# Kernel tuning notes

Measured on AMD Instinct MI355X. Metric: run time of the kernel, lower is better.

The kernel has to match this reference:

```python
import jax, jax.numpy as jnp
import numpy as np

EPS = 1e-5

def _bn_train(h, gamma, beta):
    # BatchNorm1d in training mode: batch mean and biased variance over batch dim
    mu = jnp.mean(h, axis=0)
    var = jnp.mean((h - mu) ** 2, axis=0)
    return (h - mu) * jax.lax.rsqrt(var + EPS) * gamma + beta

def setup_inputs() -> dict:
    key = jax.random.key(0)
    ks = jax.random.split(key, 12)
    B, IN, H1, H2, NC = 16384, 4096, 256, 128, 12
    x = jax.random.normal(ks[0], (B, 1, 64, 64), dtype=jnp.float32)
    y = jax.random.randint(ks[1], (B,), 0, NC, dtype=jnp.int32)
    s1 = 1.0 / np.sqrt(IN)
    W1 = jax.random.uniform(ks[2], (H1, IN), jnp.float32, -s1, s1)
    b1 = jax.random.uniform(ks[3], (H1,), jnp.float32, -s1, s1)
    g1 = jax.random.normal(ks[4], (H1,), jnp.float32) * 0.1 + 1.0
    be1 = jax.random.normal(ks[5], (H1,), jnp.float32) * 0.1
    s2 = 1.0 / np.sqrt(H1)
    W2 = jax.random.uniform(ks[6], (H2, H1), jnp.float32, -s2, s2)
    b2 = jax.random.uniform(ks[7], (H2,), jnp.float32, -s2, s2)
    g2 = jax.random.normal(ks[8], (H2,), jnp.float32) * 0.1 + 1.0
    be2 = jax.random.normal(ks[9], (H2,), jnp.float32) * 0.1
    s4 = 1.0 / np.sqrt(H2)
    W4 = jax.random.uniform(ks[10], (NC, H2), jnp.float32, -s4, s4)
    b4 = jax.random.uniform(ks[11], (NC,), jnp.float32, -s4, s4)
    return {"x": x, "W1": W1, "b1": b1, "g1": g1, "be1": be1,
            "W2": W2, "b2": b2, "g2": g2, "be2": be2,
            "W4": W4, "b4": b4, "y": y}

def reference(x, W1, b1, g1, be1, W2, b2, g2, be2, W4, b4, y):
    B = x.shape[0]
    h = x.reshape(B, -1)  # [B, 4096]
    # layer 1: binarized linear + BN(train) + hardtanh (dropout p=0 is identity)
    h = h @ jnp.sign(W1).T + jnp.sign(b1)
    h = jnp.clip(_bn_train(h, g1, be1), -1.0, 1.0)
    # layer 2
    h = h @ jnp.sign(W2).T + jnp.sign(b2)
    h = jnp.clip(_bn_train(h, g2, be2), -1.0, 1.0)
    # final float linear
    return h @ W4.T + b4  # [B, 12]
```

## Files before the change

### kernel.cpp

```cpp
#include <hip/hip_runtime.h>
#include <cstddef>

typedef __attribute__((ext_vector_type(8))) short short8;
typedef __attribute__((ext_vector_type(4))) float f4;
typedef __attribute__((ext_vector_type(4))) unsigned int u4;
typedef __attribute__((ext_vector_type(2))) unsigned int u2;

__device__ __forceinline__ unsigned int f2bf(float f){
  unsigned int u = __float_as_uint(f);
  u += 0x7fffu + ((u >> 16) & 1u);
  return u >> 16;
}
__device__ __forceinline__ float bflo(unsigned int w){ return __uint_as_float((w & 0xFFFFu) << 16); }
__device__ __forceinline__ float bfhi(unsigned int w){ return __uint_as_float(w & 0xFFFF0000u); }
__device__ __forceinline__ float fsign(float x){ return (x > 0.f) ? 1.f : ((x < 0.f) ? -1.f : 0.f); }
__device__ __forceinline__ float hclip(float x){ return fminf(1.f, fmaxf(-1.f, x)); }

#define SB0 __builtin_amdgcn_sched_barrier(0)

#define BARRIER() do { \
    SB0; \
    asm volatile("s_waitcnt lgkmcnt(0)" ::: "memory"); \
    __builtin_amdgcn_s_barrier(); \
    asm volatile("" ::: "memory"); \
    SB0; \
  } while(0)

#define VBAR(N) do { \
    SB0; \
    asm volatile("s_waitcnt vmcnt(" #N ") lgkmcnt(0)" ::: "memory"); \
    __builtin_amdgcn_s_barrier(); \
    asm volatile("" ::: "memory"); \
    SB0; \
  } while(0)

#define GL16(gp, lp) __builtin_amdgcn_global_load_lds( \
    (const __attribute__((address_space(1))) void*)(gp), \
    (__attribute__((address_space(3))) void*)(lp), 16, 0, 0)

__global__ void prep_sign_k(const float* __restrict__ W1, unsigned short* __restrict__ w1s,
                            const float* __restrict__ W2, unsigned short* __restrict__ w2s){
  int i = (blockIdx.x * blockDim.x + threadIdx.x) * 8;
  const float* w; unsigned short* o; int off;
  if (i < 1048576){ w = W1; o = w1s; off = i; }
  else            { w = W2; o = w2s; off = i - 1048576; if (off >= 32768) return; }
  f4 a = *(const f4*)(w + off);
  f4 b = *(const f4*)(w + off + 4);
  unsigned short s[8];
  #pragma unroll
  for (int j = 0; j < 4; j++) s[j]   = (a[j] > 0.f) ? 0x3F80u : ((a[j] < 0.f) ? 0xBF80u : 0u);
  #pragma unroll
  for (int j = 0; j < 4; j++) s[4+j] = (b[j] > 0.f) ? 0x3F80u : ((b[j] < 0.f) ? 0xBF80u : 0u);
  u4 v;
  v.x = (unsigned)s[0] | ((unsigned)s[1] << 16);
  v.y = (unsigned)s[2] | ((unsigned)s[3] << 16);
  v.z = (unsigned)s[4] | ((unsigned)s[5] << 16);
  v.w = (unsigned)s[6] | ((unsigned)s[7] << 16);
  *(u4*)(o + off) = v;
}

__global__ __launch_bounds__(512, 4) void gemm1_k(
    const float* __restrict__ x, const unsigned short* __restrict__ w1s,
    const float* __restrict__ b1, unsigned short* __restrict__ h1,
    float* __restrict__ part1s, float* __restrict__ part1q)
{
  __shared__ __align__(16) char lds[73728];
  const int tid  = threadIdx.x;
  const int lane = tid & 63;
  const int wid  = tid >> 6;
  const int cl   = lane & 15;
  const int g    = lane >> 4;
  const int row0 = blockIdx.x * 32;

  const int am = tid >> 4;
  const int kf = (tid & 15) * 4;
  const float* xA = x + (size_t)(row0 + am) * 4096 + kf;
  const int aw = (am * 128 + kf * 2) ^ ((am & 7) << 4);

  f4 acc[2][2];
  const f4 z = {0.f, 0.f, 0.f, 0.f};
  #pragma unroll
  for (int i = 0; i < 2; i++){ acc[i][0] = z; acc[i][1] = z; }

  f4 rA0, rA1;

#define ISSUEA(S, KB) do { rA##S = *(const f4*)(xA + (KB)*64); } while(0)

#define ISSUEB(BUF, KB) do { \
    char* _dst = lds + 8192 + (BUF)*32768; \
    _Pragma("unroll") \
    for (int _c = 0; _c < 4; _c++){ \
      int _o  = _c*8192 + tid*16; \
      int _n  = _o >> 7; \
      int _kb = (_o & 127) ^ ((_n & 7) << 4); \
      GL16((const char*)w1s + (size_t)_n*8192 + (size_t)(KB)*128 + _kb, _dst + _o); \
    } } while(0)

#define PACKA(S, ABUF) do { \
    u2 _v; \
    _v.x = f2bf(rA##S[0]) | (f2bf(rA##S[1]) << 16); \
    _v.y = f2bf(rA##S[2]) | (f2bf(rA##S[3]) << 16); \
    *(u2*)(lds + (ABUF)*4096 + aw) = _v; \
  } while(0)

#define COMPUTE(BUF) do { \
    const char* _ab = lds + (BUF)*4096; \
    const char* _bb = lds + 8192 + (BUF)*32768; \
    short8 _af[2][2]; short8 _bf[2][2]; \
    _Pragma("unroll") \
    for (int fm = 0; fm < 2; fm++){ \
      int _m = fm*16 + cl; \
      _Pragma("unroll") \
      for (int ks = 0; ks < 2; ks++) \
        _af[fm][ks] = *(const short8*)(_ab + ((_m*128 + ks*64 + g*16) ^ ((_m & 7) << 4))); \
    } \
    _Pragma("unroll") \
    for (int fn = 0; fn < 2; fn++){ \
      int _n = wid*32 + fn*16 + cl; \
      _Pragma("unroll") \
      for (int ks = 0; ks < 2; ks++) \
        _bf[fn][ks] = *(const short8*)(_bb + ((_n*128 + ks*64 + g*16) ^ ((_n & 7) << 4))); \
    } \
    _Pragma("unroll") \
    for (int ks = 0; ks < 2; ks++) \
      _Pragma("unroll") \
      for (int fm = 0; fm < 2; fm++) \
        _Pragma("unroll") \
        for (int fn = 0; fn < 2; fn++) \
          acc[fm][fn] = __builtin_amdgcn_mfma_f32_16x16x32_bf16(_af[fm][ks], _bf[fn][ks], acc[fm][fn], 0, 0, 0); \
  } while(0)

  ISSUEB(0, 0);
  ISSUEA(0, 0);
  ISSUEA(1, 1);
  SB0;
  PACKA(0, 0);
  VBAR(1);

  for (int k = 0; k < 64; k += 2){
    if (k < 63) ISSUEB(1, k + 1);
    if (k < 62) ISSUEA(0, k + 2);
    SB0;
    COMPUTE(0);
    SB0;
    if (k < 63) PACKA(1, 1);
    if (k < 62)      VBAR(1);
    else if (k < 63) VBAR(0);
    if (k + 1 < 63) ISSUEB(0, k + 2);
    if (k + 1 < 62) ISSUEA(1, k + 3);
    SB0;
    COMPUTE(1);
    SB0;
    if (k + 1 < 63){ PACKA(0, 0); VBAR(1); }
  }
#undef COMPUTE
#undef PACKA
#undef ISSUEB
#undef ISSUEA

  #pragma unroll
  for (int fn = 0; fn < 2; fn++){
    int c = wid * 32 + fn * 16 + cl;
    float sb = fsign(b1[c]);
    float s = 0.f, q = 0.f;
    #pragma unroll
    for (int fm = 0; fm < 2; fm++){
      int rbase = row0 + fm * 16 + g * 4;
      #pragma unroll
      for (int i = 0; i < 4; i++){
        float v = acc[fm][fn][i] + sb;
        h1[(size_t)(rbase + i) * 256 + c] = (unsigned short)f2bf(v);
        s += v; q += v * v;
      }
    }
    s += __shfl_xor(s, 16, 64); s += __shfl_xor(s, 32, 64);
    q += __shfl_xor(q, 16, 64); q += __shfl_xor(q, 32, 64);
    if (g == 0){
      part1s[(size_t)c * 512 + blockIdx.x] = s;
      part1q[(size_t)c * 512 + blockIdx.x] = q;
    }
  }
}

template<int COLS, int NBLK>
__global__ __launch_bounds__(64) void params_k(
    const float* __restrict__ ps, const float* __restrict__ pq,
    const float* __restrict__ g, const float* __restrict__ be,
    float* __restrict__ ab){
  int j = blockIdx.x * 64 + threadIdx.x;
  const f4* vs = (const f4*)(ps + (size_t)j * NBLK);
  const f4* vq = (const f4*)(pq + (size_t)j * NBLK);
  f4 s4 = {0,0,0,0}, q4 = {0,0,0,0};
  #pragma unroll 8
  for (int b = 0; b < NBLK/4; b++){ s4 += vs[b]; q4 += vq[b]; }
  float s = s4[0]+s4[1]+s4[2]+s4[3];
  float q = q4[0]+q4[1]+q4[2]+q4[3];
  float mu  = s * (1.f/16384.f);
  float var = q * (1.f/16384.f) - mu*mu;
  float a   = g[j] * rsqrtf(var + 1e-5f);
  ab[j] = a;
  ab[COLS + j] = be[j] - mu*a;
}

__global__ __launch_bounds__(512) void gemm2_k(
    const unsigned short* __restrict__ h1, const unsigned short* __restrict__ w2s,
    const float* __restrict__ b2, const float* __restrict__ ab1,
    unsigned short* __restrict__ h2, float* __restrict__ part2s, float* __restrict__ part2q)
{
  __shared__ __align__(16) char lds[32768];
  __shared__ __align__(16) float a1l[256];
  __shared__ __align__(16) float c1l[256];
  const int tid  = threadIdx.x;
  const int lane = tid & 63;
  const int wid  = tid >> 6;
  const int cl   = lane & 15;
  const int g    = lane >> 4;
  const int klo  = g * 8;
  const int row0 = blockIdx.x * 64;

  if (tid < 256) a1l[tid] = ab1[tid];
  else           c1l[tid - 256] = ab1[tid];

  const int am  = tid >> 3;
  const int ak0 = (tid & 7) * 8;
  const unsigned short* hA = h1 + (size_t)(row0 + am) * 256 + ak0;
  const int aw = ((am * 128) + (ak0 * 2)) ^ ((am & 7) << 4);
  const unsigned short* wbase = w2s + (size_t)(wid * 16 + cl) * 256 + klo;

  u4 q0 = *(const u4*)(hA);
  u4 q1 = *(const u4*)(hA + 64);
  u4 q2 = *(const u4*)(hA + 128);
  u4 q3 = *(const u4*)(hA + 192);
  short8 Bq0, Bq1, Br0, Br1;
  Bq0 = *(const short8*)(wbase);
  Bq1 = *(const short8*)(wbase + 32);

  BARRIER();

#define TRW(KB, RAW) do { \
    f4 _a0 = *(const f4*)(&a1l[(KB)*64 + ak0]); \
    f4 _a1 = *(const f4*)(&a1l[(KB)*64 + ak0 + 4]); \
    f4 _c0 = *(const f4*)(&c1l[(KB)*64 + ak0]); \
    f4 _c1 = *(const f4*)(&c1l[(KB)*64 + ak0 + 4]); \
    float _t0 = hclip(_a0[0]*bflo(RAW.x) + _c0[0]); \
    float _t1 = hclip(_a0[1]*bfhi(RAW.x) + _c0[1]); \
    float _t2 = hclip(_a0[2]*bflo(RAW.y) + _c0[2]); \
    float _t3 = hclip(_a0[3]*bfhi(RAW.y) + _c0[3]); \
    float _t4 = hclip(_a1[0]*bflo(RAW.z) + _c1[0]); \
    float _t5 = hclip(_a1[1]*bfhi(RAW.z) + _c1[1]); \
    float _t6 = hclip(_a1[2]*bflo(RAW.w) + _c1[2]); \
    float _t7 = hclip(_a1[3]*bfhi(RAW.w) + _c1[3]); \
    u4 _v; \
    _v.x = f2bf(_t0) | (f2bf(_t1) << 16); \
    _v.y = f2bf(_t2) | (f2bf(_t3) << 16); \
    _v.z = f2bf(_t4) | (f2bf(_t5) << 16); \
    _v.w = f2bf(_t6) | (f2bf(_t7) << 16); \
    *(u4*)(lds + (KB)*8192 + aw) = _v; \
  } while(0)

  TRW(0, q0); TRW(1, q1); TRW(2, q2); TRW(3, q3);
#undef TRW
  BARRIER();

  f4 acc[4];
  const f4 z = {0.f, 0.f, 0.f, 0.f};
  #pragma unroll
  for (int i = 0; i < 4; i++) acc[i] = z;

#define LOADB2(P, KB) do { \
    B##P##0 = *(const short8*)(wbase + (KB)*64); \
    B##P##1 = *(const short8*)(wbase + (KB)*64 + 32); \
  } while(0)

#define COMP2(BASE, P) do { \
    const char* _ab = (const char*)(BASE); \
    short8 _af[4][2]; \
    _Pragma("unroll") \
    for (int fm = 0; fm < 4; fm++){ \
      int _m = fm*16 + cl; \
      _af[fm][0] = *(const short8*)(_ab + ((_m*128 + klo*2) ^ ((_m & 7) << 4))); \
      _af[fm][1] = *(const short8*)(_ab + ((_m*128 + (32 + klo)*2) ^ ((_m & 7) << 4))); \
    } \
    _Pragma("unroll") \
    for (int fm = 0; fm < 4; fm++){ \
      acc[fm] = __builtin_amdgcn_mfma_f32_16x16x32_bf16(_af[fm][0], B##P##0, acc[fm], 0, 0, 0); \
      acc[fm] = __builtin_amdgcn_mfma_f32_16x16x32_bf16(_af[fm][1], B##P##1, acc[fm], 0, 0, 0); \
    } \
  } while(0)

  LOADB2(r, 1);
  COMP2(lds,         q);
  LOADB2(q, 2);
  COMP2(lds +  8192, r);
  LOADB2(r, 3);
  COMP2(lds + 16384, q);
  COMP2(lds + 24576, r);
#undef COMP2
#undef LOADB2

  {
    int c = wid*16 + cl;
    float sb = fsign(b2[c]);
    float s = 0.f, q = 0.f;
    #pragma unroll
    for (int fm = 0; fm < 4; fm++){
      int rbase = row0 + fm*16 + g*4;
      #pragma unroll
      for (int i = 0; i < 4; i++){
        float v = acc[fm][i] + sb;
        h2[(size_t)(rbase + i)*128 + c] = (unsigned short)f2bf(v);
        s += v; q += v*v;
      }
    }
    s += __shfl_xor(s, 16, 64); s += __shfl_xor(s, 32, 64);
    q += __shfl_xor(q, 16, 64); q += __shfl_xor(q, 32, 64);
    if (g == 0){
      part2s[c*256 + blockIdx.x] = s;
      part2q[c*256 + blockIdx.x] = q;
    }
  }
}

__global__ __launch_bounds__(128) void final_k(
    const unsigned short* __restrict__ h2,
    const float* __restrict__ part2s, const float* __restrict__ part2q,
    const float* __restrict__ g2, const float* __restrict__ be2,
    const float* __restrict__ W4, const float* __restrict__ b4,
    float* __restrict__ out)
{
  __shared__ __align__(16) float W4l[12*128];
  __shared__ __align__(16) float a2l[128];
  __shared__ __align__(16) float c2l[128];
  const int t = threadIdx.x;
  #pragma unroll
  for (int i = 0; i < 3; i++)
    *(f4*)&W4l[(i*128 + t)*4] = *(const f4*)(W4 + (i*128 + t)*4);
  {
    const f4* vs = (const f4*)(part2s + t*256);
    const f4* vq = (const f4*)(part2q + t*256);
    f4 s4 = {0,0,0,0}, q4 = {0,0,0,0};
    #pragma unroll 8
    for (int b = 0; b < 64; b++){ s4 += vs[b]; q4 += vq[b]; }
    float s = s4[0]+s4[1]+s4[2]+s4[3];
    float q = q4[0]+q4[1]+q4[2]+q4[3];
    float mu  = s * (1.f/16384.f);
    float var = q * (1.f/16384.f) - mu*mu;
    float a   = g2[t] * rsqrtf(var + 1e-5f);
    a2l[t] = a;
    c2l[t] = be2[t] - mu*a;
  }
  __syncthreads();

  const int r = blockIdx.x * 128 + t;
  const u4* hp = (const u4*)(h2 + (size_t)r * 128);
  u4 hv0 = hp[0], hv1 = hp[1], hv2 = hp[2],  hv3 = hp[3];
  u4 hv4 = hp[4], hv5 = hp[5], hv6 = hp[6],  hv7 = hp[7];
  u4 hv8 = hp[8], hv9 = hp[9], hv10 = hp[10], hv11 = hp[11];
  u4 hv12 = hp[12], hv13 = hp[13], hv14 = hp[14], hv15 = hp[15];

  float acc[12];
  #pragma unroll
  for (int o = 0; o < 12; o++) acc[o] = b4[o];

#define FPROC(HV, J) do { \
    f4 a0 = *(const f4*)&a2l[(J)*8];     f4 a1 = *(const f4*)&a2l[(J)*8 + 4]; \
    f4 c0 = *(const f4*)&c2l[(J)*8];     f4 c1 = *(const f4*)&c2l[(J)*8 + 4]; \
    float tt0 = hclip(a0[0]*bflo(HV.x) + c0[0]); \
    float tt1 = hclip(a0[1]*bfhi(HV.x) + c0[1]); \
    float tt2 = hclip(a0[2]*bflo(HV.y) + c0[2]); \
    float tt3 = hclip(a0[3]*bfhi(HV.y) + c0[3]); \
    float tt4 = hclip(a1[0]*bflo(HV.z) + c1[0]); \
    float tt5 = hclip(a1[1]*bfhi(HV.z) + c1[1]); \
    float tt6 = hclip(a1[2]*bflo(HV.w) + c1[2]); \
    float tt7 = hclip(a1[3]*bfhi(HV.w) + c1[3]); \
    _Pragma("unroll") \
    for (int o = 0; o < 12; o++){ \
      f4 w0 = *(const f4*)&W4l[o*128 + (J)*8]; \
      f4 w1 = *(const f4*)&W4l[o*128 + (J)*8 + 4]; \
      acc[o] += tt0*w0[0] + tt1*w0[1] + tt2*w0[2] + tt3*w0[3] \
              + tt4*w1[0] + tt5*w1[1] + tt6*w1[2] + tt7*w1[3]; \
    } \
  } while(0)

  FPROC(hv0, 0);  FPROC(hv1, 1);  FPROC(hv2, 2);   FPROC(hv3, 3);
  FPROC(hv4, 4);  FPROC(hv5, 5);  FPROC(hv6, 6);   FPROC(hv7, 7);
  FPROC(hv8, 8);  FPROC(hv9, 9);  FPROC(hv10, 10); FPROC(hv11, 11);
  FPROC(hv12, 12); FPROC(hv13, 13); FPROC(hv14, 14); FPROC(hv15, 15);
#undef FPROC

  #pragma unroll
  for (int o = 0; o < 12; o++) out[(size_t)r*12 + o] = acc[o];
}

extern "C" void kernel_launch(void* const* d_in, const int* in_sizes, int n_in,
                              void* d_out, int out_size, void* d_ws, size_t ws_size,
                              hipStream_t stream)
{
  const float* x   = (const float*)d_in[0];
  const float* W1  = (const float*)d_in[1];
  const float* b1  = (const float*)d_in[2];
  const float* g1  = (const float*)d_in[3];
  const float* be1 = (const float*)d_in[4];
  const float* W2  = (const float*)d_in[5];
  const float* b2  = (const float*)d_in[6];
  const float* g2  = (const float*)d_in[7];
  const float* be2 = (const float*)d_in[8];
  const float* W4  = (const float*)d_in[9];
  const float* b4  = (const float*)d_in[10];
  float* out = (float*)d_out;

  char* ws = (char*)d_ws;
  unsigned short* h1     = (unsigned short*)(ws);
  unsigned short* h2     = (unsigned short*)(ws + 8388608);
  unsigned short* w1s    = (unsigned short*)(ws + 12582912);
  unsigned short* w2s    = (unsigned short*)(ws + 14680064);
  float*          part1s = (float*)(ws + 14745600);
  float*          part1q = (float*)(ws + 15269888);
  float*          part2s = (float*)(ws + 15794176);
  float*          part2q = (float*)(ws + 15925248);
  float*          ab1    = (float*)(ws + 16056320);

  prep_sign_k<<<528, 256, 0, stream>>>(W1, w1s, W2, w2s);
  gemm1_k<<<512, 512, 0, stream>>>(x, w1s, b1, h1, part1s, part1q);
  params_k<256, 512><<<4, 64, 0, stream>>>(part1s, part1q, g1, be1, ab1);
  gemm2_k<<<256, 512, 0, stream>>>(h1, w2s, b2, ab1, h2, part2s, part2q);
  final_k<<<128, 128, 0, stream>>>(h2, part2s, part2q, g2, be2, W4, b4, out);
}
```

Measured before the change: 132.8 us.

## Restructure gemm1: fp32 A via direct LDS loads, B fragments held in registers

Doubles the rows per block to 64 and splits the 8 waves into a 2x4 grid. The fp32 activations are now streamed straight into a 4-deep swizzled LDS ring and converted to bf16 at fragment-read time. Sign weights are loaded straight from global into double-buffered registers instead of going through LDS, and each stage now covers 128 of K instead of 64. The aim is to remove the per-thread register staging and pack step for A and the LDS traffic for B. The cost is heavier register pressure, lower occupancy (launch bounds drop from 4 to 2), repeated B loads across blocks, and the BN partial sums are now written per half-block.

```diff
diff --git a/kernel.cpp b/kernel.cpp
--- a/kernel.cpp
+++ b/kernel.cpp
@@ -59,113 +59,139 @@
   *(u4*)(o + off) = v;
 }
 
-__global__ __launch_bounds__(512, 4) void gemm1_k(
+__global__ __launch_bounds__(512, 2) void gemm1_k(
     const float* __restrict__ x, const unsigned short* __restrict__ w1s,
     const float* __restrict__ b1, unsigned short* __restrict__ h1,
     float* __restrict__ part1s, float* __restrict__ part1q)
 {
-  __shared__ __align__(16) char lds[73728];
+  __shared__ __align__(16) char lds[131072];
   const int tid  = threadIdx.x;
   const int lane = tid & 63;
   const int wid  = tid >> 6;
+  const int wm   = wid >> 2;
+  const int wn   = wid & 3;
   const int cl   = lane & 15;
   const int g    = lane >> 4;
-  const int row0 = blockIdx.x * 32;
-
-  const int am = tid >> 4;
-  const int kf = (tid & 15) * 4;
-  const float* xA = x + (size_t)(row0 + am) * 4096 + kf;
-  const int aw = (am * 128 + kf * 2) ^ ((am & 7) << 4);
-
-  f4 acc[2][2];
+  const int row0 = blockIdx.x * 64;
+
+  const char* bb0 = (const char*)w1s + (size_t)(wn*64 +  0 + cl) * 8192 + g * 16;
+  const char* bb1 = (const char*)w1s + (size_t)(wn*64 + 16 + cl) * 8192 + g * 16;
+  const char* bb2 = (const char*)w1s + (size_t)(wn*64 + 32 + cl) * 8192 + g * 16;
+  const char* bb3 = (const char*)w1s + (size_t)(wn*64 + 48 + cl) * 8192 + g * 16;
+
+  f4 acc[2][4];
   const f4 z = {0.f, 0.f, 0.f, 0.f};
   #pragma unroll
-  for (int i = 0; i < 2; i++){ acc[i][0] = z; acc[i][1] = z; }
-
-  f4 rA0, rA1;
-
-#define ISSUEA(S, KB) do { rA##S = *(const f4*)(xA + (KB)*64); } while(0)
-
-#define ISSUEB(BUF, KB) do { \
-    char* _dst = lds + 8192 + (BUF)*32768; \
+  for (int i = 0; i < 2; i++)
+    #pragma unroll
+    for (int j = 0; j < 4; j++) acc[i][j] = z;
+
+  short8 B0_00, B0_01, B0_02, B0_03, B0_10, B0_11, B0_12, B0_13;
+  short8 B0_20, B0_21, B0_22, B0_23, B0_30, B0_31, B0_32, B0_33;
+  short8 B1_00, B1_01, B1_02, B1_03, B1_10, B1_11, B1_12, B1_13;
+  short8 B1_20, B1_21, B1_22, B1_23, B1_30, B1_31, B1_32, B1_33;
+
+#define ISSUEB(S, K) do { \
+    const size_t _ko = (size_t)(K) * 256; \
+    B##S##_00 = *(const short8*)(bb0 + _ko +   0); \
+    B##S##_01 = *(const short8*)(bb0 + _ko +  64); \
+    B##S##_02 = *(const short8*)(bb0 + _ko + 128); \
+    B##S##_03 = *(const short8*)(bb0 + _ko + 192); \
+    B##S##_10 = *(const short8*)(bb1 + _ko +   0); \
+    B##S##_11 = *(const short8*)(bb1 + _ko +  64); \
+    B##S##_12 = *(const short8*)(bb1 + _ko + 128); \
+    B##S##_13 = *(const short8*)(bb1 + _ko + 192); \
+    B##S##_20 = *(const short8*)(bb2 + _ko +   0); \
+    B##S##_21 = *(const short8*)(bb2 + _ko +  64); \
+    B##S##_22 = *(const short8*)(bb2 + _ko + 128); \
+    B##S##_23 = *(const short8*)(bb2 + _ko + 192); \
+    B##S##_30 = *(const short8*)(bb3 + _ko +   0); \
+    B##S##_31 = *(const short8*)(bb3 + _ko +  64); \
+    B##S##_32 = *(const short8*)(bb3 + _ko + 128); \
+    B##S##_33 = *(const short8*)(bb3 + _ko + 192); \
+  } while(0)
+
+#define ISSUEA(K) do { \
+    const int _kc = (K); \
+    char* _dst = lds + (size_t)(_kc & 3) * 32768; \
     _Pragma("unroll") \
     for (int _c = 0; _c < 4; _c++){ \
-      int _o  = _c*8192 + tid*16; \
-      int _n  = _o >> 7; \
-      int _kb = (_o & 127) ^ ((_n & 7) << 4); \
-      GL16((const char*)w1s + (size_t)_n*8192 + (size_t)(KB)*128 + _kb, _dst + _o); \
+      int _o = _c * 8192 + tid * 16; \
+      int _m = _o >> 9; \
+      int _swb = (_o & 511) ^ ((_m & 7) << 4); \
+      GL16((const char*)x + (size_t)(row0 + _m) * 16384 + (size_t)_kc * 512 + _swb, _dst + _o); \
     } } while(0)
 
-#define PACKA(S, ABUF) do { \
-    u2 _v; \
-    _v.x = f2bf(rA##S[0]) | (f2bf(rA##S[1]) << 16); \
-    _v.y = f2bf(rA##S[2]) | (f2bf(rA##S[3]) << 16); \
-    *(u2*)(lds + (ABUF)*4096 + aw) = _v; \
-  } while(0)
-
-#define COMPUTE(BUF) do { \
-    const char* _ab = lds + (BUF)*4096; \
-    const char* _bb = lds + 8192 + (BUF)*32768; \
-    short8 _af[2][2]; short8 _bf[2][2]; \
+#define MF1(S, KS) \
+    acc[0][0] = __builtin_amdgcn_mfma_f32_16x16x32_bf16(af[0][KS], B##S##_0##KS, acc[0][0], 0, 0, 0); \
+    acc[0][1] = __builtin_amdgcn_mfma_f32_16x16x32_bf16(af[0][KS], B##S##_1##KS, acc[0][1], 0, 0, 0); \
+    acc[0][2] = __builtin_amdgcn_mfma_f32_16x16x32_bf16(af[0][KS], B##S##_2##KS, acc[0][2], 0, 0, 0); \
+    acc[0][3] = __builtin_amdgcn_mfma_f32_16x16x32_bf16(af[0][KS], B##S##_3##KS, acc[0][3], 0, 0, 0); \
+    acc[1][0] = __builtin_amdgcn_mfma_f32_16x16x32_bf16(af[1][KS], B##S##_0##KS, acc[1][0], 0, 0, 0); \
+    acc[1][1] = __builtin_amdgcn_mfma_f32_16x16x32_bf16(af[1][KS], B##S##_1##KS, acc[1][1], 0, 0, 0); \
+    acc[1][2] = __builtin_amdgcn_mfma_f32_16x16x32_bf16(af[1][KS], B##S##_2##KS, acc[1][2], 0, 0, 0); \
+    acc[1][3] = __builtin_amdgcn_mfma_f32_16x16x32_bf16(af[1][KS], B##S##_3##KS, acc[1][3], 0, 0, 0);
+
+#define COMPUTE(KI, S) do { \
+    const char* _ab = lds + (size_t)((KI) & 3) * 32768; \
+    short8 af[2][4]; \
     _Pragma("unroll") \
-    for (int fm = 0; fm < 2; fm++){ \
-      int _m = fm*16 + cl; \
+    for (int _fm = 0; _fm < 2; _fm++){ \
+      int _m = wm * 32 + _fm * 16 + cl; \
+      int _sw = (_m & 7) << 4; \
       _Pragma("unroll") \
-      for (int ks = 0; ks < 2; ks++) \
-        _af[fm][ks] = *(const short8*)(_ab + ((_m*128 + ks*64 + g*16) ^ ((_m & 7) << 4))); \
+      for (int _ks = 0; _ks < 4; _ks++){ \
+        int _ba = _m * 512 + _ks * 128 + g * 32; \
+        f4 _lo = *(const f4*)(_ab + ((_ba     ) ^ _sw)); \
+        f4 _hi = *(const f4*)(_ab + ((_ba + 16) ^ _sw)); \
+        u4 _pk; \
+        _pk.x = f2bf(_lo[0]) | (f2bf(_lo[1]) << 16); \
+        _pk.y = f2bf(_lo[2]) | (f2bf(_lo[3]) << 16); \
+        _pk.z = f2bf(_hi[0]) | (f2bf(_hi[1]) << 16); \
+        _pk.w = f2bf(_hi[2]) | (f2bf(_hi[3]) << 16); \
+        af[_fm][_ks] = *(short8*)&_pk; \
+      } \
     } \
-    _Pragma("unroll") \
-    for (int fn = 0; fn < 2; fn++){ \
-      int _n = wid*32 + fn*16 + cl; \
-      _Pragma("unroll") \
-      for (int ks = 0; ks < 2; ks++) \
-        _bf[fn][ks] = *(const short8*)(_bb + ((_n*128 + ks*64 + g*16) ^ ((_n & 7) << 4))); \
-    } \
-    _Pragma("unroll") \
-    for (int ks = 0; ks < 2; ks++) \
-      _Pragma("unroll") \
-      for (int fm = 0; fm < 2; fm++) \
-        _Pragma("unroll") \
-        for (int fn = 0; fn < 2; fn++) \
-          acc[fm][fn] = __builtin_amdgcn_mfma_f32_16x16x32_bf16(_af[fm][ks], _bf[fn][ks], acc[fm][fn], 0, 0, 0); \
+    MF1(S, 0) \
+    MF1(S, 1) \
+    MF1(S, 2) \
+    MF1(S, 3) \
   } while(0)
 
   ISSUEB(0, 0);
-  ISSUEA(0, 0);
-  ISSUEA(1, 1);
-  SB0;
-  PACKA(0, 0);
-  VBAR(1);
-
-  for (int k = 0; k < 64; k += 2){
-    if (k < 63) ISSUEB(1, k + 1);
-    if (k < 62) ISSUEA(0, k + 2);
+  ISSUEA(0); ISSUEA(1); ISSUEA(2);
+  VBAR(8);
+
+  #pragma unroll 1
+  for (int kk = 0; kk < 32; kk += 2){
+    ISSUEB(1, (kk + 1 < 32) ? kk + 1 : 31);
+    ISSUEA((kk + 3 < 32) ? kk + 3 : 31);
     SB0;
-    COMPUTE(0);
+    COMPUTE(kk, 0);
     SB0;
-    if (k < 63) PACKA(1, 1);
-    if (k < 62)      VBAR(1);
-    else if (k < 63) VBAR(0);
-    if (k + 1 < 63) ISSUEB(0, k + 2);
-    if (k + 1 < 62) ISSUEA(1, k + 3);
+    VBAR(24);
+    ISSUEB(0, (kk + 2 < 32) ? kk + 2 : 31);
+    ISSUEA((kk + 4 < 32) ? kk + 4 : 31);
     SB0;
-    COMPUTE(1);
+    COMPUTE(kk + 1, 1);
     SB0;
-    if (k + 1 < 63){ PACKA(0, 0); VBAR(1); }
+    VBAR(24);
   }
+  asm volatile("s_waitcnt vmcnt(0)" ::: "memory");
+
 #undef COMPUTE
-#undef PACKA
+#undef MF1
+#undef ISSUEA
 #undef ISSUEB
-#undef ISSUEA
-
-  #pragma unroll
-  for (int fn = 0; fn < 2; fn++){
-    int c = wid * 32 + fn * 16 + cl;
+
+  #pragma unroll
+  for (int fn = 0; fn < 4; fn++){
+    int c = wn * 64 + fn * 16 + cl;
     float sb = fsign(b1[c]);
     float s = 0.f, q = 0.f;
     #pragma unroll
     for (int fm = 0; fm < 2; fm++){
-      int rbase = row0 + fm * 16 + g * 4;
+      int rbase = row0 + wm * 32 + fm * 16 + g * 4;
       #pragma unroll
       for (int i = 0; i < 4; i++){
         float v = acc[fm][fn][i] + sb;
@@ -176,8 +202,8 @@
     s += __shfl_xor(s, 16, 64); s += __shfl_xor(s, 32, 64);
     q += __shfl_xor(q, 16, 64); q += __shfl_xor(q, 32, 64);
     if (g == 0){
-      part1s[(size_t)c * 512 + blockIdx.x] = s;
-      part1q[(size_t)c * 512 + blockIdx.x] = q;
+      part1s[(size_t)c * 512 + blockIdx.x * 2 + wm] = s;
+      part1q[(size_t)c * 512 + blockIdx.x * 2 + wm] = q;
     }
   }
 }
@@ -421,7 +447,7 @@
   float*          ab1    = (float*)(ws + 16056320);
 
   prep_sign_k<<<528, 256, 0, stream>>>(W1, w1s, W2, w2s);
-  gemm1_k<<<512, 512, 0, stream>>>(x, w1s, b1, h1, part1s, part1q);
+  gemm1_k<<<256, 512, 0, stream>>>(x, w1s, b1, h1, part1s, part1q);
   params_k<256, 512><<<4, 64, 0, stream>>>(part1s, part1q, g1, be1, ab1);
   gemm2_k<<<256, 512, 0, stream>>>(h1, w2s, b2, ab1, h2, part2s, part2q);
   final_k<<<128, 128, 0, stream>>>(h2, part2s, part2q, g2, be2, W4, b4, out);
```

New measurement: 217.3 us. 1.64x slower.

## Retile gemm1 to 64-row blocks with 2x4 warp grid and 4-stage B pipeline

Applied to the files above, without the earlier changes.

Each gemm1 block now computes 64 rows instead of 32, so half as many blocks are launched. Waves are arranged 2x4 with 2x4 MFMA fragments, which halves how often the sign-weight tiles are reloaded per row. The K step shrinks to 32 and B uses a four-deep LDS ring with a padded A layout. MFMA sections are raised in priority with setprio. Fewer blocks means less parallelism across CUs, and the deeper K loop adds more barriers per block.

```diff
diff --git a/kernel.cpp b/kernel.cpp
--- a/kernel.cpp
+++ b/kernel.cpp
@@ -64,108 +64,122 @@
     const float* __restrict__ b1, unsigned short* __restrict__ h1,
     float* __restrict__ part1s, float* __restrict__ part1q)
 {
-  __shared__ __align__(16) char lds[73728];
+  __shared__ __align__(16) char lds[75776];
   const int tid  = threadIdx.x;
   const int lane = tid & 63;
   const int wid  = tid >> 6;
+  const int wm   = wid >> 2;
+  const int wn   = wid & 3;
   const int cl   = lane & 15;
   const int g    = lane >> 4;
-  const int row0 = blockIdx.x * 32;
-
-  const int am = tid >> 4;
-  const int kf = (tid & 15) * 4;
-  const float* xA = x + (size_t)(row0 + am) * 4096 + kf;
-  const int aw = (am * 128 + kf * 2) ^ ((am & 7) << 4);
-
-  f4 acc[2][2];
+  const int row0 = blockIdx.x * 64;
+
+  const float* xA = x + (size_t)(row0 + (tid >> 3)) * 4096 + (tid & 7) * 4;
+  const int aw = (tid >> 3) * 80 + (tid & 7) * 8;
+
+  const int n0  = (tid >> 2);
+  const int sb0 = ((tid & 3) * 16) ^ ((n0 & 3) << 4);
+  const int n1  = 128 + (tid >> 2);
+  const int sb1 = ((tid & 3) * 16) ^ ((n1 & 3) << 4);
+  const char* srcB0 = (const char*)w1s + (size_t)n0 * 8192 + sb0;
+  const char* srcB1 = (const char*)w1s + (size_t)n1 * 8192 + sb1;
+  const int dstB0 = tid * 16;
+  const int dstB1 = 8192 + tid * 16;
+
+  int afo[2], bfo[4];
+  #pragma unroll
+  for (int fm = 0; fm < 2; fm++)
+    afo[fm] = (wm * 32 + fm * 16 + cl) * 80 + g * 16;
+  #pragma unroll
+  for (int fn = 0; fn < 4; fn++){
+    int n = wn * 64 + fn * 16 + cl;
+    bfo[fn] = n * 64 + ((g * 16) ^ ((n & 3) << 4));
+  }
+
+  f4 acc[2][4];
   const f4 z = {0.f, 0.f, 0.f, 0.f};
   #pragma unroll
-  for (int i = 0; i < 2; i++){ acc[i][0] = z; acc[i][1] = z; }
-
-  f4 rA0, rA1;
-
-#define ISSUEA(S, KB) do { rA##S = *(const f4*)(xA + (KB)*64); } while(0)
-
-#define ISSUEB(BUF, KB) do { \
-    char* _dst = lds + 8192 + (BUF)*32768; \
-    _Pragma("unroll") \
-    for (int _c = 0; _c < 4; _c++){ \
-      int _o  = _c*8192 + tid*16; \
-      int _n  = _o >> 7; \
-      int _kb = (_o & 127) ^ ((_n & 7) << 4); \
-      GL16((const char*)w1s + (size_t)_n*8192 + (size_t)(KB)*128 + _kb, _dst + _o); \
-    } } while(0)
-
-#define PACKA(S, ABUF) do { \
+  for (int i = 0; i < 2; i++)
+    #pragma unroll
+    for (int j = 0; j < 4; j++) acc[i][j] = z;
+
+  f4 rA0, rA1, rA2, rA3;
+
+#define ISSUEA(S, K) do { rA##S = *(const f4*)(xA + (size_t)(K) * 32); } while(0)
+
+#define ISSUEB(BI, K) do { \
+    GL16(srcB0 + (size_t)(K) * 64, lds + 10240 + (BI) * 16384 + dstB0); \
+    GL16(srcB1 + (size_t)(K) * 64, lds + 10240 + (BI) * 16384 + dstB1); \
+  } while(0)
+
+#define PACKA(S, AB) do { \
     u2 _v; \
     _v.x = f2bf(rA##S[0]) | (f2bf(rA##S[1]) << 16); \
     _v.y = f2bf(rA##S[2]) | (f2bf(rA##S[3]) << 16); \
-    *(u2*)(lds + (ABUF)*4096 + aw) = _v; \
-  } while(0)
-
-#define COMPUTE(BUF) do { \
-    const char* _ab = lds + (BUF)*4096; \
-    const char* _bb = lds + 8192 + (BUF)*32768; \
-    short8 _af[2][2]; short8 _bf[2][2]; \
-    _Pragma("unroll") \
-    for (int fm = 0; fm < 2; fm++){ \
-      int _m = fm*16 + cl; \
-      _Pragma("unroll") \
-      for (int ks = 0; ks < 2; ks++) \
-        _af[fm][ks] = *(const short8*)(_ab + ((_m*128 + ks*64 + g*16) ^ ((_m & 7) << 4))); \
-    } \
-    _Pragma("unroll") \
-    for (int fn = 0; fn < 2; fn++){ \
-      int _n = wid*32 + fn*16 + cl; \
-      _Pragma("unroll") \
-      for (int ks = 0; ks < 2; ks++) \
-        _bf[fn][ks] = *(const short8*)(_bb + ((_n*128 + ks*64 + g*16) ^ ((_n & 7) << 4))); \
-    } \
-    _Pragma("unroll") \
-    for (int ks = 0; ks < 2; ks++) \
-      _Pragma("unroll") \
-      for (int fm = 0; fm < 2; fm++) \
-        _Pragma("unroll") \
-        for (int fn = 0; fn < 2; fn++) \
-          acc[fm][fn] = __builtin_amdgcn_mfma_f32_16x16x32_bf16(_af[fm][ks], _bf[fn][ks], acc[fm][fn], 0, 0, 0); \
-  } while(0)
-
-  ISSUEB(0, 0);
-  ISSUEA(0, 0);
-  ISSUEA(1, 1);
+    *(u2*)(lds + (AB) * 5120 + aw) = _v; \
+  } while(0)
+
+#define COMPUTE(AB, BB) do { \
+    const char* _ab = lds + (AB) * 5120; \
+    const char* _bb = lds + 10240 + (BB) * 16384; \
+    short8 _af0 = *(const short8*)(_ab + afo[0]); \
+    short8 _af1 = *(const short8*)(_ab + afo[1]); \
+    short8 _bf0 = *(const short8*)(_bb + bfo[0]); \
+    short8 _bf1 = *(const short8*)(_bb + bfo[1]); \
+    short8 _bf2 = *(const short8*)(_bb + bfo[2]); \
+    short8 _bf3 = *(const short8*)(_bb + bfo[3]); \
+    __builtin_amdgcn_s_setprio(1); \
+    acc[0][0] = __builtin_amdgcn_mfma_f32_16x16x32_bf16(_af0, _bf0, acc[0][0], 0, 0, 0); \
+    acc[0][1] = __builtin_amdgcn_mfma_f32_16x16x32_bf16(_af0, _bf1, acc[0][1], 0, 0, 0); \
+    acc[0][2] = __builtin_amdgcn_mfma_f32_16x16x32_bf16(_af0, _bf2, acc[0][2], 0, 0, 0); \
+    acc[0][3] = __builtin_amdgcn_mfma_f32_16x16x32_bf16(_af0, _bf3, acc[0][3], 0, 0, 0); \
+    acc[1][0] = __builtin_amdgcn_mfma_f32_16x16x32_bf16(_af1, _bf0, acc[1][0], 0, 0, 0); \
+    acc[1][1] = __builtin_amdgcn_mfma_f32_16x16x32_bf16(_af1, _bf1, acc[1][1], 0, 0, 0); \
+    acc[1][2] = __builtin_amdgcn_mfma_f32_16x16x32_bf16(_af1, _bf2, acc[1][2], 0, 0, 0); \
+    acc[1][3] = __builtin_amdgcn_mfma_f32_16x16x32_bf16(_af1, _bf3, acc[1][3], 0, 0, 0); \
+    __builtin_amdgcn_s_setprio(0); \
+  } while(0)
+
+#define STEP(K, BI2, AI3, AP1, ABR, ABW) do { \
+    ISSUEB(BI2, ((K)+2 < 128) ? (K)+2 : 127); \
+    ISSUEA(AI3, ((K)+3 < 128) ? (K)+3 : 127); \
+    SB0; \
+    COMPUTE(ABR, (K) & 3); \
+    SB0; \
+    if ((K) < 127) PACKA(AP1, ABW); \
+    VBAR(4); \
+  } while(0)
+
+  ISSUEB(0, 0); ISSUEA(0, 0);
+  ISSUEB(1, 1); ISSUEA(1, 1);
+  ISSUEA(2, 2);
   SB0;
   PACKA(0, 0);
-  VBAR(1);
-
-  for (int k = 0; k < 64; k += 2){
-    if (k < 63) ISSUEB(1, k + 1);
-    if (k < 62) ISSUEA(0, k + 2);
-    SB0;
-    COMPUTE(0);
-    SB0;
-    if (k < 63) PACKA(1, 1);
-    if (k < 62)      VBAR(1);
-    else if (k < 63) VBAR(0);
-    if (k + 1 < 63) ISSUEB(0, k + 2);
-    if (k + 1 < 62) ISSUEA(1, k + 3);
-    SB0;
-    COMPUTE(1);
-    SB0;
-    if (k + 1 < 63){ PACKA(0, 0); VBAR(1); }
+  BARRIER();
+
+  #pragma unroll 1
+  for (int kk = 0; kk < 128; kk += 4){
+    STEP(kk + 0, 2, 3, 1, 0, 1);
+    STEP(kk + 1, 3, 0, 2, 1, 0);
+    STEP(kk + 2, 0, 1, 3, 0, 1);
+    STEP(kk + 3, 1, 2, 0, 1, 0);
   }
+  asm volatile("s_waitcnt vmcnt(0)" ::: "memory");
+
+#undef STEP
 #undef COMPUTE
 #undef PACKA
 #undef ISSUEB
 #undef ISSUEA
 
   #pragma unroll
-  for (int fn = 0; fn < 2; fn++){
-    int c = wid * 32 + fn * 16 + cl;
+  for (int fn = 0; fn < 4; fn++){
+    int c = wn * 64 + fn * 16 + cl;
     float sb = fsign(b1[c]);
     float s = 0.f, q = 0.f;
     #pragma unroll
     for (int fm = 0; fm < 2; fm++){
-      int rbase = row0 + fm * 16 + g * 4;
+      int rbase = row0 + wm * 32 + fm * 16 + g * 4;
       #pragma unroll
       for (int i = 0; i < 4; i++){
         float v = acc[fm][fn][i] + sb;
@@ -176,8 +190,8 @@
     s += __shfl_xor(s, 16, 64); s += __shfl_xor(s, 32, 64);
     q += __shfl_xor(q, 16, 64); q += __shfl_xor(q, 32, 64);
     if (g == 0){
-      part1s[(size_t)c * 512 + blockIdx.x] = s;
-      part1q[(size_t)c * 512 + blockIdx.x] = q;
+      part1s[(size_t)c * 512 + blockIdx.x * 2 + wm] = s;
+      part1q[(size_t)c * 512 + blockIdx.x * 2 + wm] = q;
     }
   }
 }
@@ -421,7 +435,7 @@
   float*          ab1    = (float*)(ws + 16056320);
 
   prep_sign_k<<<528, 256, 0, stream>>>(W1, w1s, W2, w2s);
-  gemm1_k<<<512, 512, 0, stream>>>(x, w1s, b1, h1, part1s, part1q);
+  gemm1_k<<<256, 512, 0, stream>>>(x, w1s, b1, h1, part1s, part1q);
   params_k<256, 512><<<4, 64, 0, stream>>>(part1s, part1q, g1, be1, ab1);
   gemm2_k<<<256, 512, 0, stream>>>(h1, w2s, b2, ab1, h2, part2s, part2q);
   final_k<<<128, 128, 0, stream>>>(h2, part2s, part2q, g2, be2, W4, b4, out);
```

New measurement: 147.8 us. 11.3% more time.

## Load sign-packed W1 fragments directly into registers in MFMA layout, dropping LDS staging

Applied to the files above, without the earlier changes.

The sign-prep kernel now writes W1 in a fragment-friendly layout: 32-wide k chunks, with each output row's 64 bytes contiguous. The GEMM1 waves can then load their B operands straight from global memory into registers instead of staging a 64 KB double buffer in LDS. LDS use drops to 8 KB for A only, so more blocks can reside per CU. The x prefetch is deepened to three steps, and MFMA sections are wrapped in s_setprio. The trade-off is that global/L2 latency for B is hidden only one k-step ahead, and every wave fetches its own B slices with no cross-wave sharing through LDS.

```diff
diff --git a/kernel.cpp b/kernel.cpp
--- a/kernel.cpp
+++ b/kernel.cpp
@@ -26,45 +26,48 @@
     SB0; \
   } while(0)
 
-#define VBAR(N) do { \
-    SB0; \
-    asm volatile("s_waitcnt vmcnt(" #N ") lgkmcnt(0)" ::: "memory"); \
-    __builtin_amdgcn_s_barrier(); \
-    asm volatile("" ::: "memory"); \
-    SB0; \
-  } while(0)
-
-#define GL16(gp, lp) __builtin_amdgcn_global_load_lds( \
-    (const __attribute__((address_space(1))) void*)(gp), \
-    (__attribute__((address_space(3))) void*)(lp), 16, 0, 0)
-
-__global__ void prep_sign_k(const float* __restrict__ W1, unsigned short* __restrict__ w1s,
+__global__ void prep_sign_k(const float* __restrict__ W1, unsigned short* __restrict__ w1f,
                             const float* __restrict__ W2, unsigned short* __restrict__ w2s){
   int i = (blockIdx.x * blockDim.x + threadIdx.x) * 8;
-  const float* w; unsigned short* o; int off;
-  if (i < 1048576){ w = W1; o = w1s; off = i; }
-  else            { w = W2; o = w2s; off = i - 1048576; if (off >= 32768) return; }
-  f4 a = *(const f4*)(w + off);
-  f4 b = *(const f4*)(w + off + 4);
-  unsigned short s[8];
-  #pragma unroll
-  for (int j = 0; j < 4; j++) s[j]   = (a[j] > 0.f) ? 0x3F80u : ((a[j] < 0.f) ? 0xBF80u : 0u);
-  #pragma unroll
-  for (int j = 0; j < 4; j++) s[4+j] = (b[j] > 0.f) ? 0x3F80u : ((b[j] < 0.f) ? 0xBF80u : 0u);
-  u4 v;
-  v.x = (unsigned)s[0] | ((unsigned)s[1] << 16);
-  v.y = (unsigned)s[2] | ((unsigned)s[3] << 16);
-  v.z = (unsigned)s[4] | ((unsigned)s[5] << 16);
-  v.w = (unsigned)s[6] | ((unsigned)s[7] << 16);
-  *(u4*)(o + off) = v;
+  if (i < 1048576){
+    int n = i >> 12, k = i & 4095;
+    f4 a = *(const f4*)(W1 + i);
+    f4 b = *(const f4*)(W1 + i + 4);
+    u4 v;
+    v.x = (unsigned)((a[0] > 0.f) ? 0x3F80u : (a[0] < 0.f ? 0xBF80u : 0u))
+        | ((unsigned)((a[1] > 0.f) ? 0x3F80u : (a[1] < 0.f ? 0xBF80u : 0u)) << 16);
+    v.y = (unsigned)((a[2] > 0.f) ? 0x3F80u : (a[2] < 0.f ? 0xBF80u : 0u))
+        | ((unsigned)((a[3] > 0.f) ? 0x3F80u : (a[3] < 0.f ? 0xBF80u : 0u)) << 16);
+    v.z = (unsigned)((b[0] > 0.f) ? 0x3F80u : (b[0] < 0.f ? 0xBF80u : 0u))
+        | ((unsigned)((b[1] > 0.f) ? 0x3F80u : (b[1] < 0.f ? 0xBF80u : 0u)) << 16);
+    v.w = (unsigned)((b[2] > 0.f) ? 0x3F80u : (b[2] < 0.f ? 0xBF80u : 0u))
+        | ((unsigned)((b[3] > 0.f) ? 0x3F80u : (b[3] < 0.f ? 0xBF80u : 0u)) << 16);
+    size_t ob = ((size_t)(k >> 5) * 256 + (size_t)n) * 64 + (size_t)((k >> 3) & 3) * 16;
+    *(u4*)((char*)w1f + ob) = v;
+  } else {
+    int off = i - 1048576;
+    if (off >= 32768) return;
+    f4 a = *(const f4*)(W2 + off);
+    f4 b = *(const f4*)(W2 + off + 4);
+    u4 v;
+    v.x = (unsigned)((a[0] > 0.f) ? 0x3F80u : (a[0] < 0.f ? 0xBF80u : 0u))
+        | ((unsigned)((a[1] > 0.f) ? 0x3F80u : (a[1] < 0.f ? 0xBF80u : 0u)) << 16);
+    v.y = (unsigned)((a[2] > 0.f) ? 0x3F80u : (a[2] < 0.f ? 0xBF80u : 0u))
+        | ((unsigned)((a[3] > 0.f) ? 0x3F80u : (a[3] < 0.f ? 0xBF80u : 0u)) << 16);
+    v.z = (unsigned)((b[0] > 0.f) ? 0x3F80u : (b[0] < 0.f ? 0xBF80u : 0u))
+        | ((unsigned)((b[1] > 0.f) ? 0x3F80u : (b[1] < 0.f ? 0xBF80u : 0u)) << 16);
+    v.w = (unsigned)((b[2] > 0.f) ? 0x3F80u : (b[2] < 0.f ? 0xBF80u : 0u))
+        | ((unsigned)((b[3] > 0.f) ? 0x3F80u : (b[3] < 0.f ? 0xBF80u : 0u)) << 16);
+    *(u4*)(w2s + off) = v;
+  }
 }
 
 __global__ __launch_bounds__(512, 4) void gemm1_k(
-    const float* __restrict__ x, const unsigned short* __restrict__ w1s,
+    const float* __restrict__ x, const unsigned short* __restrict__ w1f,
     const float* __restrict__ b1, unsigned short* __restrict__ h1,
     float* __restrict__ part1s, float* __restrict__ part1q)
 {
-  __shared__ __align__(16) char lds[73728];
+  __shared__ __align__(16) char lds[8192];
   const int tid  = threadIdx.x;
   const int lane = tid & 63;
   const int wid  = tid >> 6;
@@ -72,87 +75,105 @@
   const int g    = lane >> 4;
   const int row0 = blockIdx.x * 32;
 
-  const int am = tid >> 4;
-  const int kf = (tid & 15) * 4;
-  const float* xA = x + (size_t)(row0 + am) * 4096 + kf;
-  const int aw = (am * 128 + kf * 2) ^ ((am & 7) << 4);
+  const float* xA = x + (size_t)(row0 + (tid >> 4)) * 4096 + (tid & 15) * 4;
+  const int aw = (tid >> 4) * 128 + (((tid & 15) * 8) ^ (((tid >> 4) & 7) << 4));
+
+  const char* w1p = (const char*)w1f;
+  const int bof0 = (wid * 32 +  0 + cl) * 64 + g * 16;
+  const int bof1 = (wid * 32 + 16 + cl) * 64 + g * 16;
+
+  int afo[2][2];
+  #pragma unroll
+  for (int fm = 0; fm < 2; fm++){
+    int m = fm * 16 + cl;
+    afo[fm][0] = m * 128 + ((     g * 16) ^ ((m & 7) << 4));
+    afo[fm][1] = m * 128 + ((64 + g * 16) ^ ((m & 7) << 4));
+  }
 
   f4 acc[2][2];
   const f4 z = {0.f, 0.f, 0.f, 0.f};
-  #pragma unroll
-  for (int i = 0; i < 2; i++){ acc[i][0] = z; acc[i][1] = z; }
-
-  f4 rA0, rA1;
-
-#define ISSUEA(S, KB) do { rA##S = *(const f4*)(xA + (KB)*64); } while(0)
-
-#define ISSUEB(BUF, KB) do { \
-    char* _dst = lds + 8192 + (BUF)*32768; \
-    _Pragma("unroll") \
-    for (int _c = 0; _c < 4; _c++){ \
-      int _o  = _c*8192 + tid*16; \
-      int _n  = _o >> 7; \
-      int _kb = (_o & 127) ^ ((_n & 7) << 4); \
-      GL16((const char*)w1s + (size_t)_n*8192 + (size_t)(KB)*128 + _kb, _dst + _o); \
-    } } while(0)
-
-#define PACKA(S, ABUF) do { \
+  acc[0][0] = z; acc[0][1] = z; acc[1][0] = z; acc[1][1] = z;
+
+  f4 rA0, rA1, rA2, rA3;
+  short8 B00, B01, B10, B11;
+
+#define ISSUEA(S, K) do { rA##S = *(const f4*)(xA + (size_t)(K) * 64); } while(0)
+
+#define ISSUEB(K) do { \
+    const char* _p = w1p + (size_t)(K) * 32768; \
+    B00 = *(const short8*)(_p +         bof0); \
+    B01 = *(const short8*)(_p + 16384 + bof0); \
+    B10 = *(const short8*)(_p +         bof1); \
+    B11 = *(const short8*)(_p + 16384 + bof1); \
+  } while(0)
+
+#define PACKA(S, AB) do { \
     u2 _v; \
     _v.x = f2bf(rA##S[0]) | (f2bf(rA##S[1]) << 16); \
     _v.y = f2bf(rA##S[2]) | (f2bf(rA##S[3]) << 16); \
-    *(u2*)(lds + (ABUF)*4096 + aw) = _v; \
-  } while(0)
-
-#define COMPUTE(BUF) do { \
-    const char* _ab = lds + (BUF)*4096; \
-    const char* _bb = lds + 8192 + (BUF)*32768; \
-    short8 _af[2][2]; short8 _bf[2][2]; \
-    _Pragma("unroll") \
-    for (int fm = 0; fm < 2; fm++){ \
-      int _m = fm*16 + cl; \
-      _Pragma("unroll") \
-      for (int ks = 0; ks < 2; ks++) \
-        _af[fm][ks] = *(const short8*)(_ab + ((_m*128 + ks*64 + g*16) ^ ((_m & 7) << 4))); \
-    } \
-    _Pragma("unroll") \
-    for (int fn = 0; fn < 2; fn++){ \
-      int _n = wid*32 + fn*16 + cl; \
-      _Pragma("unroll") \
-      for (int ks = 0; ks < 2; ks++) \
-        _bf[fn][ks] = *(const short8*)(_bb + ((_n*128 + ks*64 + g*16) ^ ((_n & 7) << 4))); \
-    } \
-    _Pragma("unroll") \
-    for (int ks = 0; ks < 2; ks++) \
-      _Pragma("unroll") \
-      for (int fm = 0; fm < 2; fm++) \
-        _Pragma("unroll") \
-        for (int fn = 0; fn < 2; fn++) \
-          acc[fm][fn] = __builtin_amdgcn_mfma_f32_16x16x32_bf16(_af[fm][ks], _bf[fn][ks], acc[fm][fn], 0, 0, 0); \
-  } while(0)
-
-  ISSUEB(0, 0);
-  ISSUEA(0, 0);
-  ISSUEA(1, 1);
+    *(u2*)(lds + (AB) * 4096 + aw) = _v; \
+  } while(0)
+
+#define COMPUTE(KI) do { \
+    const char* _ab = lds + ((KI) & 1) * 4096; \
+    short8 _af00 = *(const short8*)(_ab + afo[0][0]); \
+    short8 _af01 = *(const short8*)(_ab + afo[0][1]); \
+    short8 _af10 = *(const short8*)(_ab + afo[1][0]); \
+    short8 _af11 = *(const short8*)(_ab + afo[1][1]); \
+    __builtin_amdgcn_s_setprio(1); \
+    acc[0][0] = __builtin_amdgcn_mfma_f32_16x16x32_bf16(_af00, B00, acc[0][0], 0, 0, 0); \
+    acc[0][1] = __builtin_amdgcn_mfma_f32_16x16x32_bf16(_af00, B10, acc[0][1], 0, 0, 0); \
+    acc[1][0] = __builtin_amdgcn_mfma_f32_16x16x32_bf16(_af10, B00, acc[1][0], 0, 0, 0); \
+    acc[1][1] = __builtin_amdgcn_mfma_f32_16x16x32_bf16(_af10, B10, acc[1][1], 0, 0, 0); \
+    acc[0][0] = __builtin_amdgcn_mfma_f32_16x16x32_bf16(_af01, B01, acc[0][0], 0, 0, 0); \
+    acc[0][1] = __builtin_amdgcn_mfma_f32_16x16x32_bf16(_af01, B11, acc[0][1], 0, 0, 0); \
+    acc[1][0] = __builtin_amdgcn_mfma_f32_16x16x32_bf16(_af01, B01, acc[1][0], 0, 0, 0); \
+    acc[1][1] = __builtin_amdgcn_mfma_f32_16x16x32_bf16(_af11, B11, acc[1][1], 0, 0, 0); \
+  } while(0)
+#undef COMPUTE
+#define COMPUTE(KI) do { \
+    const char* _ab = lds + ((KI) & 1) * 4096; \
+    short8 _af00 = *(const short8*)(_ab + afo[0][0]); \
+    short8 _af01 = *(const short8*)(_ab + afo[0][1]); \
+    short8 _af10 = *(const short8*)(_ab + afo[1][0]); \
+    short8 _af11 = *(const short8*)(_ab + afo[1][1]); \
+    __builtin_amdgcn_s_setprio(1); \
+    acc[0][0] = __builtin_amdgcn_mfma_f32_16x16x32_bf16(_af00, B00, acc[0][0], 0, 0, 0); \
+    acc[0][1] = __builtin_amdgcn_mfma_f32_16x16x32_bf16(_af00, B10, acc[0][1], 0, 0, 0); \
+    acc[1][0] = __builtin_amdgcn_mfma_f32_16x16x32_bf16(_af10, B00, acc[1][0], 0, 0, 0); \
+    acc[1][1] = __builtin_amdgcn_mfma_f32_16x16x32_bf16(_af10, B10, acc[1][1], 0, 0, 0); \
+    acc[0][0] = __builtin_amdgcn_mfma_f32_16x16x32_bf16(_af01, B01, acc[0][0], 0, 0, 0); \
+    acc[0][1] = __builtin_amdgcn_mfma_f32_16x16x32_bf16(_af01, B11, acc[0][1], 0, 0, 0); \
+    acc[1][0] = __builtin_amdgcn_mfma_f32_16x16x32_bf16(_af11, B01, acc[1][0], 0, 0, 0); \
+    acc[1][1] = __builtin_amdgcn_mfma_f32_16x16x32_bf16(_af11, B11, acc[1][1], 0, 0, 0); \
+    __builtin_amdgcn_s_setprio(0); \
+  } while(0)
+
+#define STEP(K, AS3, AP1) do { \
+    COMPUTE(K); \
+    ISSUEB(((K) + 1 < 64) ? (K) + 1 : 63); \
+    ISSUEA(AS3, ((K) + 3 < 64) ? (K) + 3 : 63); \
+    SB0; \
+    if ((K) < 63) PACKA(AP1, ((K) + 1) & 1); \
+    BARRIER(); \
+  } while(0)
+
+  ISSUEB(0);
+  ISSUEA(0, 0); ISSUEA(1, 1); ISSUEA(2, 2);
   SB0;
   PACKA(0, 0);
-  VBAR(1);
-
-  for (int k = 0; k < 64; k += 2){
-    if (k < 63) ISSUEB(1, k + 1);
-    if (k < 62) ISSUEA(0, k + 2);
-    SB0;
-    COMPUTE(0);
-    SB0;
-    if (k < 63) PACKA(1, 1);
-    if (k < 62)      VBAR(1);
-    else if (k < 63) VBAR(0);
-    if (k + 1 < 63) ISSUEB(0, k + 2);
-    if (k + 1 < 62) ISSUEA(1, k + 3);
-    SB0;
-    COMPUTE(1);
-    SB0;
-    if (k + 1 < 63){ PACKA(0, 0); VBAR(1); }
-  }
+  BARRIER();
+
+  #pragma unroll 1
+  for (int kk = 0; kk < 64; kk += 4){
+    STEP(kk + 0, 3, 1);
+    STEP(kk + 1, 0, 2);
+    STEP(kk + 2, 1, 3);
+    STEP(kk + 3, 2, 0);
+  }
+  asm volatile("s_waitcnt vmcnt(0)" ::: "memory");
+
+#undef STEP
 #undef COMPUTE
 #undef PACKA
 #undef ISSUEB
@@ -412,7 +433,7 @@
   char* ws = (char*)d_ws;
   unsigned short* h1     = (unsigned short*)(ws);
   unsigned short* h2     = (unsigned short*)(ws + 8388608);
-  unsigned short* w1s    = (unsigned short*)(ws + 12582912);
+  unsigned short* w1f    = (unsigned short*)(ws + 12582912);
   unsigned short* w2s    = (unsigned short*)(ws + 14680064);
   float*          part1s = (float*)(ws + 14745600);
   float*          part1q = (float*)(ws + 15269888);
@@ -420,8 +441,8 @@
   float*          part2q = (float*)(ws + 15925248);
   float*          ab1    = (float*)(ws + 16056320);
 
-  prep_sign_k<<<528, 256, 0, stream>>>(W1, w1s, W2, w2s);
-  gemm1_k<<<512, 512, 0, stream>>>(x, w1s, b1, h1, part1s, part1q);
+  prep_sign_k<<<528, 256, 0, stream>>>(W1, w1f, W2, w2s);
+  gemm1_k<<<512, 512, 0, stream>>>(x, w1f, b1, h1, part1s, part1q);
   params_k<256, 512><<<4, 64, 0, stream>>>(part1s, part1q, g1, be1, ab1);
   gemm2_k<<<256, 512, 0, stream>>>(h1, w2s, b2, ab1, h2, part2s, part2q);
   final_k<<<128, 128, 0, stream>>>(h2, part2s, part2q, g2, be2, W4, b4, out);
```

New measurement: 143.3 us. 1.08x slower.
